# Kernel tuning notes

Measured on AMD Instinct MI355X. Metric: run time of the kernel, lower is better.

## Reference

```python
import jax, jax.numpy as jnp
import numpy as np

HIDDEN = 2048
HEADS = 16
HEAD_DIM = HIDDEN // HEADS
BATCH = 2
SEQ = 2048
LN_EPS = 1e-5


def setup_inputs() -> dict:
    key = jax.random.key(0)
    ks = jax.random.split(key, 14)
    g = 0.02  # xavier gain used in _init_weights
    lim = g * np.sqrt(6.0 / (HIDDEN + HIDDEN))
    def lin_w(k):
        return jax.random.uniform(k, (HIDDEN, HIDDEN), jnp.float32, -lim, lim)
    inp = {
        "hidden_states": jax.random.normal(ks[0], (BATCH, SEQ, HIDDEN), jnp.float32),
        "cross_states": jax.random.normal(ks[1], (BATCH, SEQ, HIDDEN), jnp.float32),
        "Wq": lin_w(ks[2]), "bq": jnp.zeros((HIDDEN,), jnp.float32),
        "Wk": lin_w(ks[3]), "bk": jnp.zeros((HIDDEN,), jnp.float32),
        "Wv": lin_w(ks[4]), "bv": jnp.zeros((HIDDEN,), jnp.float32),
        "Wo": lin_w(ks[5]), "bo": jnp.zeros((HIDDEN,), jnp.float32),
        "Wg": jax.random.uniform(ks[6], (HIDDEN, HIDDEN), jnp.float32, -np.sqrt(6.0/(2*HIDDEN)), np.sqrt(6.0/(2*HIDDEN))),
        "bg": jnp.zeros((HIDDEN,), jnp.float32),
        "ln_gamma": jnp.ones((HIDDEN,), jnp.float32),
        "ln_beta": jnp.zeros((HIDDEN,), jnp.float32),
    }
    return inp


def reference(hidden_states, cross_states, Wq, bq, Wk, bk, Wv, bv, Wo, bo, Wg, bg, ln_gamma, ln_beta):
    B, S, H = hidden_states.shape
    scale = HEAD_DIM ** -0.5
    # projections (weights stored as [in, out]; equivalent to torch x @ W.T with W.T pre-applied)
    q = hidden_states @ Wq + bq
    k = cross_states @ Wk + bk
    v = cross_states @ Wv + bv
    # [B, S, H] -> [B, heads, S, head_dim]
    def split_heads(x):
        return x.reshape(B, -1, HEADS, HEAD_DIM).transpose(0, 2, 1, 3)
    q, k, v = split_heads(q), split_heads(k), split_heads(v)
    scores = jnp.einsum('bhqd,bhkd->bhqk', q, k) * scale
    probs = jax.nn.softmax(scores, axis=-1)
    attn = jnp.einsum('bhqk,bhkd->bhqd', probs, v)
    attn = attn.transpose(0, 2, 1, 3).reshape(B, -1, H)
    attn = attn @ Wo + bo
    gate = jax.nn.sigmoid(hidden_states @ Wg + bg)
    attn = gate * attn  # dropout rate 0 -> identity
    out = hidden_states + attn
    mu = jnp.mean(out, axis=-1, keepdims=True)
    var = jnp.mean(jnp.square(out - mu), axis=-1, keepdims=True)
    out = (out - mu) * jax.lax.rsqrt(var + LN_EPS) * ln_gamma + ln_beta
    return out
```

## Files before the change

### kernel.cpp

```cpp
#include <hip/hip_runtime.h>

typedef __bf16 bf16;
typedef bf16 bf16x8 __attribute__((ext_vector_type(8)));
typedef bf16 bf16x4 __attribute__((ext_vector_type(4)));
typedef float floatx4 __attribute__((ext_vector_type(4)));

#define HID 2048
#define MROWS 4096

__device__ __forceinline__ void gload_lds16(const bf16* g, bf16* l) {
    __builtin_amdgcn_global_load_lds((const __attribute__((address_space(1))) void*)g,
                                     (__attribute__((address_space(3))) void*)l, 16, 0, 0);
}

__global__ __launch_bounds__(256) void convert2_kernel(const float* __restrict__ X0, const float* __restrict__ X1,
                                                       bf16* __restrict__ Y0, bf16* __restrict__ Y1)
{
    const float* X = blockIdx.z ? X1 : X0;
    bf16* Y = blockIdx.z ? Y1 : Y0;
    const int i = (blockIdx.x * 256 + threadIdx.x) * 4;
    const float4 v = *(const float4*)(X + i);
    bf16x4 o;
    o[0] = (bf16)v.x; o[1] = (bf16)v.y; o[2] = (bf16)v.z; o[3] = (bf16)v.w;
    *(bf16x4*)(Y + i) = o;
}

__global__ __launch_bounds__(256) void transpose5_kernel(
    const float* __restrict__ W0, const float* __restrict__ W1, const float* __restrict__ W2,
    const float* __restrict__ W3, const float* __restrict__ W4,
    bf16* __restrict__ T0, bf16* __restrict__ T1, bf16* __restrict__ T2,
    bf16* __restrict__ T3, bf16* __restrict__ T4)
{
    const float* W; bf16* WT;
    switch (blockIdx.z) {
        case 0: W = W0; WT = T0; break;
        case 1: W = W1; WT = T1; break;
        case 2: W = W2; WT = T2; break;
        case 3: W = W3; WT = T3; break;
        default: W = W4; WT = T4; break;
    }
    __shared__ float tile[32][33];
    const int n0 = blockIdx.x * 32, k0 = blockIdx.y * 32;
    const int tx = threadIdx.x & 31, ty = threadIdx.x >> 5;
    #pragma unroll
    for (int r = 0; r < 32; r += 8)
        tile[ty + r][tx] = W[(size_t)(k0 + ty + r) * HID + n0 + tx];
    __syncthreads();
    #pragma unroll
    for (int r = 0; r < 32; r += 8)
        WT[(size_t)(n0 + ty + r) * HID + k0 + tx] = (bf16)tile[tx][ty + r];
}

__global__ __launch_bounds__(256) void transpose_v_kernel(const bf16* __restrict__ X, bf16* __restrict__ Y)
{
    __shared__ bf16 tile[32][33];
    const int b = blockIdx.z;
    const int c0 = blockIdx.x * 32, t0 = blockIdx.y * 32;
    const int tx = threadIdx.x & 31, ty = threadIdx.x >> 5;
    const bf16* Xb = X + (size_t)b * HID * HID;
    bf16* Yb = Y + (size_t)b * HID * HID;
    #pragma unroll
    for (int r = 0; r < 32; r += 8)
        tile[ty + r][tx] = Xb[(size_t)(t0 + ty + r) * HID + c0 + tx];
    __syncthreads();
    #pragma unroll
    for (int r = 0; r < 32; r += 8)
        Yb[(size_t)(c0 + ty + r) * HID + t0 + tx] = tile[tx][ty + r];
}

#define BAR() __builtin_amdgcn_s_barrier()
#define WAIT_LGKM0() asm volatile("s_waitcnt lgkmcnt(0)" ::: "memory")
#define WAIT_VM(N) asm volatile("s_waitcnt vmcnt(" #N ")" ::: "memory")

#define READ_A(SLOT) do { \
    _Pragma("unroll") \
    for (int mf = 0; mf < 4; mf++) \
      _Pragma("unroll") \
      for (int ks = 0; ks < 2; ks++) \
        af[mf][ks] = *(const bf16x8*)((SLOT) + (wm + mf * 16 + l15) * 64 + (((ks * 4 + quad) ^ swz) * 8)); \
    } while (0)

#define READ_B(DST, SLOT) do { \
    _Pragma("unroll") \
    for (int nf = 0; nf < 2; nf++) \
      _Pragma("unroll") \
      for (int ks = 0; ks < 2; ks++) \
        DST[nf][ks] = *(const bf16x8*)((SLOT) + (wn + nf * 16 + l15) * 64 + (((ks * 4 + quad) ^ swz) * 8)); \
    } while (0)

#define STAGE_A(DSTSLOT, ROWOFF, KT) do { \
    gload_lds16(Asrc + (size_t)(ROWOFF) * HID + (KT),        (DSTSLOT) + ldsOff); \
    gload_lds16(Asrc + (size_t)((ROWOFF) + 64) * HID + (KT), (DSTSLOT) + ldsOff + 4096); } while (0)

#define STAGE_B(DSTSLOT, ROWOFF, KT) do { \
    gload_lds16(Bsrc + (size_t)(ROWOFF) * HID + (KT),        (DSTSLOT) + ldsOff); \
    gload_lds16(Bsrc + (size_t)((ROWOFF) + 64) * HID + (KT), (DSTSLOT) + ldsOff + 4096); } while (0)

#define MFMA_QUAD(BF, MH, NH) \
    __builtin_amdgcn_s_setprio(1); \
    _Pragma("unroll") \
    for (int ks = 0; ks < 2; ks++) \
      _Pragma("unroll") \
      for (int mf = 0; mf < 4; mf++) \
        _Pragma("unroll") \
        for (int nf = 0; nf < 2; nf++) \
          acc[(MH) * 4 + mf][(NH) * 2 + nf] = __builtin_amdgcn_mfma_f32_16x16x32_bf16( \
              af[mf][ks], BF[nf][ks], acc[(MH) * 4 + mf][(NH) * 2 + nf], 0, 0, 0); \
    __builtin_amdgcn_s_setprio(0);

__global__ __launch_bounds__(512, 2) void gemm_qgkv256_kernel(
    const bf16* __restrict__ H, const bf16* __restrict__ Cx,
    const bf16* __restrict__ Wqg, const bf16* __restrict__ Wkv,
    const float* __restrict__ bq, const float* __restrict__ bg,
    const float* __restrict__ bk, const float* __restrict__ bv,
    bf16* __restrict__ qo, bf16* __restrict__ go,
    bf16* __restrict__ ko, bf16* __restrict__ vo)
{
    constexpr int BK = 64;
    constexpr int NT = HID / BK;
    __shared__ __align__(16) bf16 Ar[4][128 * BK];
    __shared__ __align__(16) bf16 Br[4][128 * BK];

    const int z = blockIdx.z;
    const bf16* A  = z ? Cx : H;
    const bf16* BT = z ? Wkv : Wqg;
    const int tid = threadIdx.x;
    const int wave = tid >> 6, lane = tid & 63;
    const int m0 = blockIdx.x * 256, n0 = blockIdx.y * 256;
    const int wm = (wave & 1) * 64;
    const int wn = (wave >> 1) * 32;
    const int l15 = lane & 15, quad = lane >> 4;
    const int swz = l15 & 7;

    floatx4 acc[8][4] = {};

    const int hrow = tid >> 3;
    const int cc0  = (tid & 7) ^ (hrow & 7);
    const bf16* Asrc = A  + (size_t)(m0 + hrow) * HID + cc0 * 8;
    const bf16* Bsrc = BT + (size_t)(n0 + hrow) * HID + cc0 * 8;
    const int ldsOff = tid * 8;

    STAGE_A(Ar[0], 0,   0);
    STAGE_B(Br[0], 0,   0);
    STAGE_A(Ar[1], 128, 0);
    STAGE_B(Br[1], 128, 0);
    STAGE_A(Ar[2], 0,   BK);
    STAGE_B(Br[2], 0,   BK);
    WAIT_VM(4); BAR();

    bf16x8 af[4][2], bl[2][2], bh[2][2];
    READ_B(bl, Br[0]);

    for (int t = 0; t < NT; t++) {
        const int sw = (t & 1) << 1;
        bf16* a_lo   = Ar[sw];
        bf16* a_hi   = Ar[sw | 1];
        bf16* b_hi   = Br[sw | 1];
        bf16* a_hi_n = Ar[(sw | 1) ^ 2];
        bf16* b_hi_n = Br[(sw | 1) ^ 2];
        bf16* b_lo_n = Br[sw ^ 2];
        const int kt1 = (t + 1) * BK, kt2 = (t + 2) * BK;
        const bool g1 = (t + 1 < NT), g2 = (t + 2 < NT);

        READ_A(a_lo);
        if (g1) STAGE_A(a_hi_n, 128, kt1);
        BAR(); WAIT_LGKM0();
        MFMA_QUAD(bl, 0, 0);
        WAIT_VM(6); BAR();

        READ_B(bh, b_hi);
        if (g1) STAGE_B(b_hi_n, 128, kt1);
        BAR(); WAIT_LGKM0();
        MFMA_QUAD(bh, 0, 1);
        WAIT_VM(6); BAR();

        READ_A(a_hi);
        if (g2) STAGE_A(Ar[sw], 0, kt2);
        BAR(); WAIT_LGKM0();
        MFMA_QUAD(bl, 1, 0);
        WAIT_VM(6); BAR();

        if (g1) READ_B(bl, b_lo_n);
        if (g2) STAGE_B(Br[sw], 0, kt2);
        BAR(); WAIT_LGKM0();
        MFMA_QUAD(bh, 1, 1);
        WAIT_VM(6); BAR();
    }

    const bool half2 = (n0 >= HID);
    const float* bias = z ? (half2 ? bv : bk) : (half2 ? bg : bq);
    bf16* C = z ? (half2 ? vo : ko) : (half2 ? go : qo);
    const bool sig = (!z) && half2;
    const int nb = n0 - (half2 ? HID : 0);
    #pragma unroll
    for (int nh = 0; nh < 2; nh++)
    #pragma unroll
    for (int nf = 0; nf < 2; nf++) {
        const int col = nb + nh * 128 + wn + nf * 16 + l15;
        const float bvv = bias[col];
        #pragma unroll
        for (int mh = 0; mh < 2; mh++)
        #pragma unroll
        for (int mf = 0; mf < 4; mf++) {
            #pragma unroll
            for (int r = 0; r < 4; r++) {
                const int row = m0 + mh * 128 + wm + mf * 16 + quad * 4 + r;
                float val = acc[mh * 4 + mf][nh * 2 + nf][r] + bvv;
                if (sig) val = 1.0f / (1.0f + __expf(-val));
                C[(size_t)row * HID + col] = (bf16)val;
            }
        }
    }
}

__global__ __launch_bounds__(256) void gemm_bt_kernel(const bf16* __restrict__ A, const bf16* __restrict__ BT,
                                                      const float* __restrict__ bias, bf16* __restrict__ C)
{
    constexpr int BK = 64;
    __shared__ __align__(16) bf16 As[128 * BK];
    __shared__ __align__(16) bf16 Bs[128 * BK];
    const int tid = threadIdx.x;
    const int wave = tid >> 6, lane = tid & 63;
    const int m0 = blockIdx.x * 128, n0 = blockIdx.y * 128;
    const int wm = (wave & 1) * 64, wn = (wave >> 1) * 64;
    const int l15 = lane & 15, q = lane >> 4;
    const int swz = l15 & 7;
    floatx4 acc[4][4] = {};
    const int srow = tid >> 3;
    const int scc = ((tid & 7) ^ (srow & 7)) * 8;
    const bf16* Ag = A  + (size_t)(m0 + srow) * HID + scc;
    const bf16* Bg = BT + (size_t)(n0 + srow) * HID + scc;
    bf16* Asl = As + tid * 8;
    bf16* Bsl = Bs + tid * 8;

    for (int kt = 0; kt < HID; kt += BK) {
        __syncthreads();
        #pragma unroll
        for (int rr = 0; rr < 4; rr++) {
            gload_lds16(Ag + (size_t)(rr * 32) * HID + kt, Asl + rr * 2048);
            gload_lds16(Bg + (size_t)(rr * 32) * HID + kt, Bsl + rr * 2048);
        }
        __syncthreads();
        #pragma unroll
        for (int ks = 0; ks < 2; ks++) {
            const int cc = (ks * 4 + q) ^ swz;
            bf16x8 af[4], bfr[4];
            #pragma unroll
            for (int i = 0; i < 4; i++)
                af[i] = *(const bf16x8*)(As + (wm + i * 16 + l15) * 64 + cc * 8);
            #pragma unroll
            for (int j = 0; j < 4; j++)
                bfr[j] = *(const bf16x8*)(Bs + (wn + j * 16 + l15) * 64 + cc * 8);
            #pragma unroll
            for (int i = 0; i < 4; i++)
                #pragma unroll
                for (int j = 0; j < 4; j++)
                    acc[i][j] = __builtin_amdgcn_mfma_f32_16x16x32_bf16(af[i], bfr[j], acc[i][j], 0, 0, 0);
        }
    }
    #pragma unroll
    for (int j = 0; j < 4; j++) {
        const int col = n0 + wn + j * 16 + l15;
        const float bvv = bias[col];
        #pragma unroll
        for (int i = 0; i < 4; i++) {
            #pragma unroll
            for (int r = 0; r < 4; r++) {
                const int row = m0 + wm + i * 16 + q * 4 + r;
                C[(size_t)row * HID + col] = (bf16)(acc[i][j][r] + bvv);
            }
        }
    }
}

__global__ __launch_bounds__(256) void attention_mfma4_kernel(const bf16* __restrict__ Q, const bf16* __restrict__ K,
                                                              const bf16* __restrict__ Vt,
                                                              bf16* __restrict__ Op0, bf16* __restrict__ Op1,
                                                              float* __restrict__ lp0, float* __restrict__ lp1)
{
    constexpr int PP = 72;
    __shared__ __align__(16) bf16 Ks[64 * 128];
    __shared__ __align__(16) bf16 Vts[128 * 64];
    __shared__ __align__(16) bf16 Ps[128 * PP];

    const int tid = threadIdx.x;
    const int wave = tid >> 6, lane = tid & 63;
    const int l15 = lane & 15, quad = lane >> 4;
    const int swz = l15 & 7;
    const int b = blockIdx.x >> 4, h = blockIdx.x & 15;
    const int q0 = blockIdx.y * 128;
    const int kt0 = blockIdx.z * 1024;
    bf16* Op = blockIdx.z ? Op1 : Op0;
    float* lp = blockIdx.z ? lp1 : lp0;
    const bf16* Qg = Q + (size_t)(b * 2048) * HID + h * 128;
    const bf16* Kg = K + (size_t)b * 2048 * HID + h * 128;
    const bf16* Vg = Vt + (size_t)(b * 2048 + h * 128) * HID;

    const int wq0 = wave * 32;

    const float qsc = 0.08838834764831845f * 1.44269504f;
    bf16x8 qreg[2][4];
    #pragma unroll
    for (int s = 0; s < 2; s++)
        #pragma unroll
        for (int kk = 0; kk < 4; kk++) {
            bf16x8 t = *(const bf16x8*)(Qg + (size_t)(q0 + wq0 + s * 16 + l15) * HID + kk * 32 + quad * 8);
            #pragma unroll
            for (int e = 0; e < 8; e++) t[e] = (bf16)((float)t[e] * qsc);
            qreg[s][kk] = t;
        }

    const int krow = tid >> 4;
    const int kcc = ((tid & 15) ^ (krow & 7)) * 8;
    const bf16* KgS = Kg + (size_t)krow * HID + kcc;
    bf16* Ksl = Ks + tid * 8;
    const int vrow = tid >> 3;
    const int vcc = ((tid & 7) ^ (vrow & 7)) * 8;
    const bf16* VgS = Vg + (size_t)vrow * HID + vcc;
    bf16* Vsl = Vts + tid * 8;

    float lsum[2] = {0.f, 0.f};
    floatx4 oacc[2][8] = {};

    for (int kt = kt0; kt < kt0 + 1024; kt += 64) {
        __syncthreads();
        #pragma unroll
        for (int rr = 0; rr < 4; rr++) {
            gload_lds16(KgS + (size_t)(kt + rr * 16) * HID, Ksl + rr * 2048);
            gload_lds16(VgS + (size_t)(rr * 32) * HID + kt, Vsl + rr * 2048);
        }
        __syncthreads();

        floatx4 sacc[4][2];
        #pragma unroll
        for (int j = 0; j < 4; j++)
            #pragma unroll
            for (int s = 0; s < 2; s++) sacc[j][s] = (floatx4){0.f, 0.f, 0.f, 0.f};
        #pragma unroll
        for (int kk = 0; kk < 4; kk++) {
            const int cc = (kk * 4 + quad) ^ swz;
            #pragma unroll
            for (int j = 0; j < 4; j++) {
                const bf16x8 kf = *(const bf16x8*)(Ks + (j * 16 + l15) * 128 + cc * 8);
                #pragma unroll
                for (int s = 0; s < 2; s++)
                    sacc[j][s] = __builtin_amdgcn_mfma_f32_16x16x32_bf16(kf, qreg[s][kk], sacc[j][s], 0, 0, 0);
            }
        }

        #pragma unroll
        for (int s = 0; s < 2; s++) {
            const int prow = wq0 + s * 16 + l15;
            float ps = 0.f;
            #pragma unroll
            for (int j = 0; j < 4; j++) {
                bf16x4 pw;
                #pragma unroll
                for (int r = 0; r < 4; r++) {
                    const float p = exp2f(sacc[j][s][r]);
                    ps += p;
                    pw[r] = (bf16)p;
                }
                *(bf16x4*)(Ps + prow * PP + j * 16 + quad * 4) = pw;
            }
            lsum[s] += ps;
        }
        #pragma unroll
        for (int ks = 0; ks < 2; ks++) {
            const int cc = (ks * 4 + quad) ^ swz;
            bf16x8 pf[2];
            #pragma unroll
            for (int s = 0; s < 2; s++)
                pf[s] = *(const bf16x8*)(Ps + (wq0 + s * 16 + l15) * PP + ks * 32 + quad * 8);
            #pragma unroll
            for (int dt = 0; dt < 8; dt++) {
                const bf16x8 vf = *(const bf16x8*)(Vts + (dt * 16 + l15) * 64 + cc * 8);
                #pragma unroll
                for (int s = 0; s < 2; s++)
                    oacc[s][dt] = __builtin_amdgcn_mfma_f32_16x16x32_bf16(pf[s], vf, oacc[s][dt], 0, 0, 0);
            }
        }
    }

    #pragma unroll
    for (int s = 0; s < 2; s++) {
        float l = lsum[s];
        l += __shfl_xor(l, 16);
        l += __shfl_xor(l, 32);
        if (quad == 0)
            lp[(size_t)(b * 2048 + q0 + wq0 + s * 16 + l15) * 16 + h] = l;
        #pragma unroll
        for (int r = 0; r < 4; r++) {
            const size_t row = (size_t)(b * 2048 + q0 + wq0 + s * 16 + quad * 4 + r);
            #pragma unroll
            for (int dt = 0; dt < 8; dt++)
                Op[row * HID + h * 128 + dt * 16 + l15] = (bf16)(oacc[s][dt][r]);
        }
    }
}

__global__ __launch_bounds__(256) void attn_combine_kernel(const bf16* __restrict__ O0, const bf16* __restrict__ O1,
                                                           const float* __restrict__ l0, const float* __restrict__ l1,
                                                           bf16* __restrict__ out)
{
    const int row = blockIdx.x;
    const int c0 = threadIdx.x * 8;
    const int h = c0 >> 7;
    const size_t base = (size_t)row * HID;
    const float inv = 1.f / (l0[row * 16 + h] + l1[row * 16 + h]);
    const bf16x8 a = *(const bf16x8*)(O0 + base + c0);
    const bf16x8 c = *(const bf16x8*)(O1 + base + c0);
    bf16x8 o;
    #pragma unroll
    for (int e = 0; e < 8; e++) o[e] = (bf16)(((float)a[e] + (float)c[e]) * inv);
    *(bf16x8*)(out + base + c0) = o;
}

__global__ __launch_bounds__(256) void ln_kernel(const float* __restrict__ hidden, const bf16* __restrict__ gate,
                                                 const bf16* __restrict__ attnp, const float* __restrict__ gamma,
                                                 const float* __restrict__ beta, float* __restrict__ out)
{
    __shared__ float red[4];
    __shared__ float red2[4];
    const int row = blockIdx.x;
    const int tid = threadIdx.x;
    const size_t base = (size_t)row * HID;
    const int c0 = tid * 8;
    const float4 h0 = *(const float4*)(hidden + base + c0);
    const float4 h1 = *(const float4*)(hidden + base + c0 + 4);
    const bf16x8 g = *(const bf16x8*)(gate + base + c0);
    const bf16x8 a = *(const bf16x8*)(attnp + base + c0);
    float t[8] = {h0.x, h0.y, h0.z, h0.w, h1.x, h1.y, h1.z, h1.w};
    float sum = 0.f;
    #pragma unroll
    for (int e = 0; e < 8; e++) { t[e] += (float)g[e] * (float)a[e]; sum += t[e]; }
    #pragma unroll
    for (int o = 1; o < 64; o <<= 1) sum += __shfl_xor(sum, o);
    const int wave = tid >> 6, lane = tid & 63;
    if (lane == 0) red[wave] = sum;
    __syncthreads();
    const float mu = (red[0] + red[1] + red[2] + red[3]) * (1.f / HID);
    float vs = 0.f;
    #pragma unroll
    for (int e = 0; e < 8; e++) { const float d = t[e] - mu; vs += d * d; }
    #pragma unroll
    for (int o = 1; o < 64; o <<= 1) vs += __shfl_xor(vs, o);
    if (lane == 0) red2[wave] = vs;
    __syncthreads();
    const float var = (red2[0] + red2[1] + red2[2] + red2[3]) * (1.f / HID);
    const float inv = rsqrtf(var + 1e-5f);
    float res[8];
    #pragma unroll
    for (int e = 0; e < 8; e++) res[e] = (t[e] - mu) * inv * gamma[c0 + e] + beta[c0 + e];
    *(float4*)(out + base + c0)     = make_float4(res[0], res[1], res[2], res[3]);
    *(float4*)(out + base + c0 + 4) = make_float4(res[4], res[5], res[6], res[7]);
}

extern "C" void kernel_launch(void* const* d_in, const int* in_sizes, int n_in,
                              void* d_out, int out_size, void* d_ws, size_t ws_size,
                              hipStream_t stream) {
    const float* hidden = (const float*)d_in[0];
    const float* cross  = (const float*)d_in[1];
    const float* Wq = (const float*)d_in[2];
    const float* bq = (const float*)d_in[3];
    const float* Wk = (const float*)d_in[4];
    const float* bk = (const float*)d_in[5];
    const float* Wv = (const float*)d_in[6];
    const float* bv = (const float*)d_in[7];
    const float* Wo = (const float*)d_in[8];
    const float* bo = (const float*)d_in[9];
    const float* Wg = (const float*)d_in[10];
    const float* bg = (const float*)d_in[11];
    const float* gamma = (const float*)d_in[12];
    const float* beta  = (const float*)d_in[13];
    float* out = (float*)d_out;

    char* ws = (char*)d_ws;
    const size_t MB = 1ull << 20;
    bf16* hbf  = (bf16*)(ws);
    bf16* cbf  = (bf16*)(ws + 16 * MB);
    bf16* WqgT = (bf16*)(ws + 32 * MB);
    bf16* WkvT = (bf16*)(ws + 48 * MB);
    bf16* WoT  = (bf16*)(ws + 64 * MB);
    bf16* qbf  = (bf16*)(ws + 72 * MB);
    bf16* kbf  = (bf16*)(ws + 88 * MB);
    bf16* vbf  = (bf16*)(ws + 104 * MB);
    bf16* gbf  = (bf16*)(ws + 120 * MB);
    bf16* abf  = (bf16*)(ws + 136 * MB);
    bf16* WgTp = WqgT + (size_t)HID * HID;
    bf16* WvTp = WkvT + (size_t)HID * HID;
    bf16* vtr  = cbf;
    bf16* Op0  = hbf;
    bf16* Op1  = WqgT;
    float* l0  = (float*)WkvT;
    float* l1  = (float*)((char*)WkvT + 1 * MB);
    bf16* pbf  = qbf;

    convert2_kernel<<<dim3(8192, 1, 2), 256, 0, stream>>>(hidden, cross, hbf, cbf);
    transpose5_kernel<<<dim3(64, 64, 5), 256, 0, stream>>>(Wq, Wg, Wk, Wv, Wo, WqgT, WgTp, WkvT, WvTp, WoT);
    gemm_qgkv256_kernel<<<dim3(16, 16, 2), 512, 0, stream>>>(hbf, cbf, WqgT, WkvT, bq, bg, bk, bv,
                                                             qbf, gbf, kbf, vbf);
    transpose_v_kernel<<<dim3(64, 64, 2), 256, 0, stream>>>(vbf, vtr);
    attention_mfma4_kernel<<<dim3(32, 16, 2), 256, 0, stream>>>(qbf, kbf, vtr, Op0, Op1, l0, l1);
    attn_combine_kernel<<<MROWS, 256, 0, stream>>>(Op0, Op1, l0, l1, abf);
    gemm_bt_kernel<<<dim3(32, 16), 256, 0, stream>>>(abf, WoT, bo, pbf);
    ln_kernel<<<MROWS, 256, 0, stream>>>(hidden, gbf, pbf, gamma, beta, out);
}
```

Baseline: 483.1 us.

## Deepen QGKV GEMM prefetch to full two-tile lookahead and remap blocks across XCDs

New measurement: 532.1 us. 10.1% more time.

```diff
diff --git a/kernel.cpp b/kernel.cpp
--- a/kernel.cpp
+++ b/kernel.cpp
@@ -121,12 +121,15 @@
     __shared__ __align__(16) bf16 Ar[4][128 * BK];
     __shared__ __align__(16) bf16 Br[4][128 * BK];
 
-    const int z = blockIdx.z;
-    const bf16* A  = z ? Cx : H;
-    const bf16* BT = z ? Wkv : Wqg;
+    const int flat = blockIdx.x + (blockIdx.y << 4) + (blockIdx.z << 8);
+    const int nw = (flat & 7) * 64 + (flat >> 3);
+    const int bx = nw & 15, by = (nw >> 4) & 15, bz = nw >> 8;
+
+    const bf16* A  = bz ? Cx : H;
+    const bf16* BT = bz ? Wkv : Wqg;
     const int tid = threadIdx.x;
     const int wave = tid >> 6, lane = tid & 63;
-    const int m0 = blockIdx.x * 256, n0 = blockIdx.y * 256;
+    const int m0 = bx * 256, n0 = by * 256;
     const int wm = (wave & 1) * 64;
     const int wn = (wave >> 1) * 32;
     const int l15 = lane & 15, quad = lane >> 4;
@@ -142,55 +145,80 @@
 
     STAGE_A(Ar[0], 0,   0);
     STAGE_B(Br[0], 0,   0);
+    STAGE_B(Br[1], 128, 0);
     STAGE_A(Ar[1], 128, 0);
-    STAGE_B(Br[1], 128, 0);
+    STAGE_B(Br[2], 0,   BK);
     STAGE_A(Ar[2], 0,   BK);
-    STAGE_B(Br[2], 0,   BK);
-    WAIT_VM(4); BAR();
+    STAGE_B(Br[3], 128, BK);
+    STAGE_A(Ar[3], 128, BK);
+    WAIT_VM(8); BAR();
 
     bf16x8 af[4][2], bl[2][2], bh[2][2];
     READ_B(bl, Br[0]);
 
-    for (int t = 0; t < NT; t++) {
+    READ_A(Ar[0]);
+    BAR(); WAIT_LGKM0();
+    MFMA_QUAD(bl, 0, 0);
+    BAR();
+
+    READ_B(bh, Br[1]);
+    STAGE_B(Br[0], 0, 2 * BK);
+    STAGE_A(Ar[0], 0, 2 * BK);
+    BAR(); WAIT_LGKM0();
+    MFMA_QUAD(bh, 0, 1);
+    WAIT_VM(6); BAR();
+
+    READ_A(Ar[1]);
+    STAGE_B(Br[1], 128, 2 * BK);
+    BAR(); WAIT_LGKM0();
+    MFMA_QUAD(bl, 1, 0);
+    BAR();
+
+    READ_B(bl, Br[2]);
+    STAGE_A(Ar[1], 128, 2 * BK);
+    BAR(); WAIT_LGKM0();
+    MFMA_QUAD(bh, 1, 1);
+    BAR();
+
+    for (int t = 1; t < NT; t++) {
         const int sw = (t & 1) << 1;
-        bf16* a_lo   = Ar[sw];
-        bf16* a_hi   = Ar[sw | 1];
-        bf16* b_hi   = Br[sw | 1];
-        bf16* a_hi_n = Ar[(sw | 1) ^ 2];
-        bf16* b_hi_n = Br[(sw | 1) ^ 2];
+        bf16* a_lo = Ar[sw];
+        bf16* a_hi = Ar[sw | 1];
+        bf16* b_lo = Br[sw];
+        bf16* b_hi = Br[sw | 1];
         bf16* b_lo_n = Br[sw ^ 2];
-        const int kt1 = (t + 1) * BK, kt2 = (t + 2) * BK;
+        const int kt2 = (t + 2) * BK;
         const bool g1 = (t + 1 < NT), g2 = (t + 2 < NT);
 
         READ_A(a_lo);
-        if (g1) STAGE_A(a_hi_n, 128, kt1);
+        if (g2) STAGE_B(b_lo, 0, kt2);
         BAR(); WAIT_LGKM0();
         MFMA_QUAD(bl, 0, 0);
-        WAIT_VM(6); BAR();
+        BAR();
 
         READ_B(bh, b_hi);
-        if (g1) STAGE_B(b_hi_n, 128, kt1);
+        if (g2) STAGE_A(a_lo, 0, kt2);
         BAR(); WAIT_LGKM0();
         MFMA_QUAD(bh, 0, 1);
         WAIT_VM(6); BAR();
 
         READ_A(a_hi);
-        if (g2) STAGE_A(Ar[sw], 0, kt2);
+        if (g2) STAGE_B(b_hi, 128, kt2);
         BAR(); WAIT_LGKM0();
         MFMA_QUAD(bl, 1, 0);
-        WAIT_VM(6); BAR();
+        BAR();
 
         if (g1) READ_B(bl, b_lo_n);
-        if (g2) STAGE_B(Br[sw], 0, kt2);
+        if (g2) STAGE_A(a_hi, 128, kt2);
         BAR(); WAIT_LGKM0();
         MFMA_QUAD(bh, 1, 1);
-        WAIT_VM(6); BAR();
+        BAR();
     }
 
     const bool half2 = (n0 >= HID);
-    const float* bias = z ? (half2 ? bv : bk) : (half2 ? bg : bq);
-    bf16* C = z ? (half2 ? vo : ko) : (half2 ? go : qo);
-    const bool sig = (!z) && half2;
+    const float* bias = bz ? (half2 ? bv : bk) : (half2 ? bg : bq);
+    bf16* C = bz ? (half2 ? vo : ko) : (half2 ? go : qo);
+    const bool sig = (!bz) && half2;
     const int nb = n0 - (half2 ? HID : 0);
     #pragma unroll
     for (int nh = 0; nh < 2; nh++)
```
